# Performance work log

Measured on AMD Instinct MI355X. Metric: run time of the kernel, lower is better.

Reference implementation:

```python
import jax, jax.numpy as jnp
import numpy as np


def setup_inputs() -> dict:
    key = jax.random.key(0)
    k0, k1, k2, k3, k4, k5 = jax.random.split(key, 6)
    L1, L2, B, D = 512, 512, 32, 1024
    inputs1 = jax.random.normal(k0, (L1, B, D), dtype=jnp.float32)
    inputs2 = jax.random.normal(k1, (L2, B, D), dtype=jnp.float32)
    # mask value 0 marks a valid token (module keeps pairs where both masks == 0)
    mask1 = jax.random.randint(k2, (L1, B), 0, 2, dtype=jnp.int64)
    mask2 = jax.random.randint(k3, (L2, B), 0, 2, dtype=jnp.int64)
    W = jax.random.normal(k4, (D, D), dtype=jnp.float32) * 0.02
    b = jax.random.normal(k5, (1,), dtype=jnp.float32) * 0.02
    return {"inputs1": inputs1, "inputs2": inputs2, "mask1": mask1,
            "mask2": mask2, "W": W, "b": b, "k": 256}


def reference(inputs1, inputs2, mask1, mask2, W, b, k):
    # inputs: [len, bsz, hdim]; masks: [len, bsz]
    H1 = jnp.transpose(inputs1, (1, 0, 2))  # [B, L1, D]
    H2 = jnp.transpose(inputs2, (1, 0, 2))  # [B, L2, D]
    # bilinear scores: H1 @ W @ H2^T + b, then relu  -> [B, L1, L2]
    S = jax.nn.relu(jnp.einsum('bid,de,bje->bij', H1, W, H2) + b[0])
    # pair is valid iff both mask entries are 0
    valid = (mask1.T[:, :, None] == 0) & (mask2.T[:, None, :] == 0)  # [B, L1, L2]
    B = S.shape[0]
    S_flat = jnp.where(valid.reshape(B, -1), S.reshape(B, -1), -jnp.inf)
    num_elems = S_flat.shape[1]
    k_actual = min(k, num_elems)
    q, _ = jax.lax.top_k(S_flat, k_actual)  # [B, k_actual]
    # replace -inf tail entries with the last finite value in each row
    neg = jnp.isneginf(q)
    q_num_finite = k_actual - neg.sum(axis=-1)  # [B]
    fill = jnp.take_along_axis(q, (q_num_finite - 1)[:, None], axis=1)  # [B, 1]
    q = jnp.where(neg, fill, q)
    if k_actual < k:
        q = jnp.concatenate(
            [q, jnp.broadcast_to(q[:, -1:], (B, k - k_actual))], axis=1)
    return q
```

## Files before the change

kernel.cpp:

```cpp
#include <hip/hip_runtime.h>

typedef __bf16 bf16_t;
typedef bf16_t bf16x8 __attribute__((ext_vector_type(8)));
typedef float floatx4 __attribute__((ext_vector_type(4)));

#define L1C 512
#define L2C 512
#define BC  32
#define DC  1024
#define KTOP 256
#define NBIN 4096
#define CAP  1024
#define FBUF 16384

__device__ __forceinline__ unsigned short f2bf(float f) {
    unsigned u = __float_as_uint(f);
    u += 0x7FFFu + ((u >> 16) & 1u);
    return (unsigned short)(u >> 16);
}

__device__ __forceinline__ void g2l16(const unsigned short* g, unsigned short* l) {
    __builtin_amdgcn_global_load_lds((const unsigned int*)g, (unsigned int*)l,
                                     16, 0, 0);
}

__device__ __forceinline__ float decode_key(unsigned k) {
    return __uint_as_float(k & 0x7FFFFFFFu);
}

__global__ __launch_bounds__(256) void cast_tr_kernel(
    const float* __restrict__ in1, const float* __restrict__ in2,
    unsigned short* __restrict__ A1, unsigned short* __restrict__ A2) {
    int r = blockIdx.x;
    const float* src;
    unsigned short* dst;
    if (r < L1C * BC) {
        int l = r >> 5, b = r & 31;
        src = in1 + (size_t)r * DC;
        dst = A1 + ((size_t)b * L1C + l) * DC;
    } else {
        int r2 = r - L1C * BC;
        int l = r2 >> 5, b = r2 & 31;
        src = in2 + (size_t)r2 * DC;
        dst = A2 + ((size_t)b * L2C + l) * DC;
    }
    int t = threadIdx.x;
    float4 v = reinterpret_cast<const float4*>(src)[t];
    ushort4 o;
    o.x = f2bf(v.x); o.y = f2bf(v.y); o.z = f2bf(v.z); o.w = f2bf(v.w);
    reinterpret_cast<ushort4*>(dst)[t] = o;
}

__global__ void transpose_cast_kernel(const float* __restrict__ W,
                                      unsigned short* __restrict__ Wt) {
    __shared__ float tile[32][33];
    int d0 = blockIdx.x * 32, e0 = blockIdx.y * 32;
    int tx = threadIdx.x;
    for (int i = threadIdx.y; i < 32; i += 8)
        tile[i][tx] = W[(size_t)(d0 + i) * DC + e0 + tx];
    __syncthreads();
    for (int i = threadIdx.y; i < 32; i += 8)
        Wt[(size_t)(e0 + i) * DC + d0 + tx] = f2bf(tile[tx][i]);
}

__global__ void init_kernel(const int* __restrict__ mask1,
                            const int* __restrict__ mask2,
                            int* __restrict__ m1t, int* __restrict__ m2t,
                            unsigned* __restrict__ cnt) {
    int gid = blockIdx.x * blockDim.x + threadIdx.x;
    if (gid < L1C * BC) {
        int l = gid & 511, b = gid >> 9;
        m1t[gid] = mask1[(l << 5) + b];
        m2t[gid] = mask2[(l << 5) + b];
    }
    if (gid < BC * 16) cnt[gid] = 0;
}

__global__ __launch_bounds__(256) void gemm1_kernel(
    const unsigned short* __restrict__ A,
    const unsigned short* __restrict__ Bt,
    unsigned short* __restrict__ C) {
    __shared__ unsigned short As[128][32];
    __shared__ unsigned short Bs[128][32];
    int tid = threadIdx.x;
    int wave = tid >> 6, lane = tid & 63;
    int lane15 = lane & 15, quad = lane >> 4;
    int wm = wave >> 1, wn = wave & 1;
    size_t m0 = (size_t)blockIdx.x * 128, n0 = (size_t)blockIdx.y * 128;

    floatx4 zero = {0.f, 0.f, 0.f, 0.f};
    floatx4 acc[4][4];
#pragma unroll
    for (int i = 0; i < 4; i++)
#pragma unroll
        for (int j = 0; j < 4; j++) acc[i][j] = zero;

    for (int k0 = 0; k0 < DC; k0 += 32) {
#pragma unroll
        for (int c = 0; c < 2; c++) {
            int cid = c * 256 + tid;
            int row = cid >> 2, col8 = (cid & 3) * 8;
            unsigned short* lbase = &As[0][0] + (c * 256 + wave * 64) * 8;
            g2l16(&A[(m0 + row) * DC + k0 + col8], lbase);
            unsigned short* lbase2 = &Bs[0][0] + (c * 256 + wave * 64) * 8;
            g2l16(&Bt[(n0 + row) * DC + k0 + col8], lbase2);
        }
        __syncthreads();
        bf16x8 af[4], bfr[4];
#pragma unroll
        for (int mi = 0; mi < 4; mi++)
            af[mi] = *reinterpret_cast<const bf16x8*>(&As[wm * 64 + mi * 16 + lane15][quad * 8]);
#pragma unroll
        for (int ni = 0; ni < 4; ni++)
            bfr[ni] = *reinterpret_cast<const bf16x8*>(&Bs[wn * 64 + ni * 16 + lane15][quad * 8]);
#pragma unroll
        for (int mi = 0; mi < 4; mi++)
#pragma unroll
            for (int ni = 0; ni < 4; ni++)
                acc[mi][ni] = __builtin_amdgcn_mfma_f32_16x16x32_bf16(
                    af[mi], bfr[ni], acc[mi][ni], 0, 0, 0);
        __syncthreads();
    }
#pragma unroll
    for (int mi = 0; mi < 4; mi++)
#pragma unroll
        for (int ni = 0; ni < 4; ni++)
#pragma unroll
            for (int r = 0; r < 4; r++) {
                size_t row = m0 + wm * 64 + mi * 16 + quad * 4 + r;
                size_t col = n0 + wn * 64 + ni * 16 + lane15;
                C[row * DC + col] = f2bf(acc[mi][ni][r]);
            }
}

__global__ __launch_bounds__(256) void gemm2_kernel(
    const unsigned short* __restrict__ Tm,
    const unsigned short* __restrict__ H2,
    const int* __restrict__ m1t, const int* __restrict__ m2t,
    const float* __restrict__ bptr,
    unsigned* __restrict__ cand,
    unsigned* __restrict__ cnt) {
    __shared__ unsigned short As[128][32];
    __shared__ unsigned short Bs[128][32];
    __shared__ unsigned lh[NBIN];
    __shared__ unsigned csum[256];
    __shared__ int m1s[128], m2s[128];
    __shared__ unsigned tsh, lcnt;
    int tid = threadIdx.x;
    int wave = tid >> 6, lane = tid & 63;
    int lane15 = lane & 15, quad = lane >> 4;
    int wm = wave >> 1, wn = wave & 1;
    int L = blockIdx.x;
    int xcd = L & 7, tile = (L >> 3) & 15, chunk = L >> 7;
    int b = xcd + (chunk << 3);
    int bx = tile & 3, by = tile >> 2;
    int m0 = bx * 128, n0 = by * 128;
    int gblk = b * 16 + by * 4 + bx;
    const unsigned short* Ab = Tm + (size_t)b * L1C * DC;
    const unsigned short* Bb = H2 + (size_t)b * L2C * DC;

    for (int i = tid; i < NBIN; i += 256) lh[i] = 0;
    if (tid < 128) m1s[tid] = (m1t[b * L1C + m0 + tid] == 0);
    else           m2s[tid - 128] = (m2t[b * L2C + n0 + tid - 128] == 0);

    floatx4 zero = {0.f, 0.f, 0.f, 0.f};
    floatx4 acc[4][4];
#pragma unroll
    for (int i = 0; i < 4; i++)
#pragma unroll
        for (int j = 0; j < 4; j++) acc[i][j] = zero;

    for (int k0 = 0; k0 < DC; k0 += 32) {
#pragma unroll
        for (int c = 0; c < 2; c++) {
            int cid = c * 256 + tid;
            int row = cid >> 2, col8 = (cid & 3) * 8;
            unsigned short* lbase = &As[0][0] + (c * 256 + wave * 64) * 8;
            g2l16(&Ab[(size_t)(m0 + row) * DC + k0 + col8], lbase);
            unsigned short* lbase2 = &Bs[0][0] + (c * 256 + wave * 64) * 8;
            g2l16(&Bb[(size_t)(n0 + row) * DC + k0 + col8], lbase2);
        }
        __syncthreads();
        bf16x8 af[4], bfr[4];
#pragma unroll
        for (int mi = 0; mi < 4; mi++)
            af[mi] = *reinterpret_cast<const bf16x8*>(&As[wm * 64 + mi * 16 + lane15][quad * 8]);
#pragma unroll
        for (int ni = 0; ni < 4; ni++)
            bfr[ni] = *reinterpret_cast<const bf16x8*>(&Bs[wn * 64 + ni * 16 + lane15][quad * 8]);
#pragma unroll
        for (int mi = 0; mi < 4; mi++)
#pragma unroll
            for (int ni = 0; ni < 4; ni++)
                acc[mi][ni] = __builtin_amdgcn_mfma_f32_16x16x32_bf16(
                    af[mi], bfr[ni], acc[mi][ni], 0, 0, 0);
        __syncthreads();
    }

    float bias = bptr[0];
    unsigned zc = 0;
#pragma unroll
    for (int ni = 0; ni < 4; ni++) {
        int jl = wn * 64 + ni * 16 + lane15;
        int v2 = m2s[jl];
#pragma unroll
        for (int mi = 0; mi < 4; mi++)
#pragma unroll
            for (int r = 0; r < 4; r++) {
                int il = wm * 64 + mi * 16 + quad * 4 + r;
                float s = acc[mi][ni][r] + bias;
                if (v2 && m1s[il]) {
                    if (s > 0.f)
                        atomicAdd(&lh[(__float_as_uint(s) | 0x80000000u) >> 20], 1u);
                    else
                        zc++;
                }
            }
    }
    if (zc) atomicAdd(&lh[2048], zc);
    __syncthreads();
    unsigned s16 = 0;
#pragma unroll
    for (int i = 0; i < 16; i++) s16 += lh[tid * 16 + i];
    csum[tid] = s16;
    __syncthreads();
    if (tid == 0) {
        unsigned cum = 0, bin = 2048;
        int found = 0;
        for (int c = 255; c >= 128 && !found; --c) {
            unsigned cs = csum[c];
            if (cum + cs >= KTOP) {
                for (int bb = c * 16 + 15; bb >= c * 16; --bb) {
                    unsigned h = lh[bb];
                    if (cum + h >= KTOP) { bin = (unsigned)bb; found = 1; break; }
                    cum += h;
                }
            } else cum += cs;
        }
        tsh = bin << 20;
        lcnt = 0;
    }
    __syncthreads();
    unsigned T = tsh;
    unsigned base = (unsigned)gblk * CAP;
#pragma unroll
    for (int ni = 0; ni < 4; ni++) {
        int jl = wn * 64 + ni * 16 + lane15;
        int v2 = m2s[jl];
#pragma unroll
        for (int mi = 0; mi < 4; mi++)
#pragma unroll
            for (int r = 0; r < 4; r++) {
                int il = wm * 64 + mi * 16 + quad * 4 + r;
                float s = acc[mi][ni][r] + bias;
                s = s > 0.f ? s : 0.f;
                unsigned key = (v2 && m1s[il])
                                   ? (__float_as_uint(s) | 0x80000000u) : 0u;
                if (key >= T) {
                    unsigned p = atomicAdd(&lcnt, 1u);
                    if (p < CAP) cand[base + p] = key;
                }
            }
    }
    __syncthreads();
    if (tid == 0) cnt[gblk] = lcnt < CAP ? lcnt : CAP;
}

__global__ __launch_bounds__(1024) void final_kernel(
    const unsigned* __restrict__ cand, const unsigned* __restrict__ cnt,
    float* __restrict__ out) {
    __shared__ unsigned buf[FBUF];
    __shared__ unsigned h[NBIN];
    __shared__ unsigned ss[256];
    __shared__ unsigned scnt_s[16], off_s[16];
    __shared__ unsigned ntot_s, sel_c, sel_a, B_s, R_s, mcount;
    __shared__ int have_s;
    __shared__ unsigned srt[256];
    int b = blockIdx.x, tid = threadIdx.x;

    if (tid < 16) {
        unsigned c = cnt[b * 16 + tid];
        scnt_s[tid] = c < CAP ? c : CAP;
    }
    __syncthreads();
    if (tid == 0) {
        unsigned o = 0;
        for (int i = 0; i < 16; i++) { off_s[i] = o; o += scnt_s[i]; }
        ntot_s = o;
        have_s = 1;
    }
    __syncthreads();
    for (int blk = 0; blk < 16; blk++) {
        unsigned c = scnt_s[blk], o = off_s[blk];
        const unsigned* p = cand + (size_t)(b * 16 + blk) * CAP;
        for (unsigned i = tid; i < c; i += 1024) buf[o + i] = p[i];
    }
    __syncthreads();
    unsigned n = ntot_s;

    unsigned Kr = KTOP;
    unsigned pfx = 0;
    unsigned kth = 0;
    for (int pass = 0; pass < 3; pass++) {
        int bins = (pass < 2) ? NBIN : 256;
        int shift = (pass == 0) ? 20 : (pass == 1) ? 8 : 0;
        int nch = bins >> 4;
        for (int i = tid; i < bins; i += 1024) h[i] = 0;
        __syncthreads();
        for (unsigned i = tid; i < n; i += 1024) {
            unsigned k = buf[i];
            bool ok = (pass == 0) ||
                      (pass == 1 && (k >> 20) == pfx) ||
                      (pass == 2 && (k >> 8) == pfx);
            if (ok) atomicAdd(&h[(k >> shift) & (bins - 1)], 1u);
        }
        __syncthreads();
        if (tid < nch) {
            unsigned s = 0;
#pragma unroll
            for (int i = 0; i < 16; i++) s += h[tid * 16 + i];
            ss[tid] = s;
        }
        __syncthreads();
        for (int off = 1; off < nch; off <<= 1) {
            unsigned v = 0;
            if (tid < nch && tid + (unsigned)off < (unsigned)nch) v = ss[tid + off];
            __syncthreads();
            if (tid < nch) ss[tid] += v;
            __syncthreads();
        }
        if (pass == 0) {
            if (tid == 0) have_s = (ss[0] >= KTOP);
            __syncthreads();
            if (!have_s) break;
        }
        if (tid < nch) {
            unsigned above = (tid + 1 < (unsigned)nch) ? ss[tid + 1] : 0u;
            if (above < Kr && ss[tid] >= Kr) { sel_c = tid; sel_a = above; }
        }
        __syncthreads();
        if (tid == 0) {
            unsigned cum = sel_a;
            for (int bb = (int)sel_c * 16 + 15; bb >= (int)sel_c * 16; --bb) {
                unsigned hb = h[bb];
                if (cum + hb >= Kr) { B_s = (unsigned)bb; R_s = Kr - cum; break; }
                cum += hb;
            }
        }
        __syncthreads();
        unsigned Bv = B_s;
        Kr = R_s;
        if (pass == 0) pfx = Bv;
        else if (pass == 1) pfx = (pfx << 12) | Bv;
        else kth = (pfx << 8) | Bv;
        __syncthreads();
    }

    if (tid == 0) mcount = 0;
    __syncthreads();
    int have = have_s;
    unsigned lim = have ? kth : 0u;
    for (unsigned i = tid; i < n; i += 1024) {
        unsigned k = buf[i];
        if (k > lim) {
            unsigned p = atomicAdd(&mcount, 1u);
            if (p < 256) srt[p] = k;
        }
    }
    __syncthreads();
    unsigned m = mcount;
    if (tid < 256 && tid >= (int)m) srt[tid] = have ? kth : 0u;
    for (int k2 = 2; k2 <= 256; k2 <<= 1) {
        for (int j2 = k2 >> 1; j2 > 0; j2 >>= 1) {
            __syncthreads();
            if (tid < 256) {
                int ixj = tid ^ j2;
                if (ixj > tid) {
                    unsigned a = srt[tid], c = srt[ixj];
                    bool up = (tid & k2) == 0;
                    if (up ? (a < c) : (a > c)) { srt[tid] = c; srt[ixj] = a; }
                }
            }
        }
    }
    __syncthreads();
    if (tid < 256) {
        unsigned nval = have ? KTOP : (m < KTOP ? m : KTOP);
        float v;
        if ((unsigned)tid < nval) v = decode_key(srt[tid]);
        else v = (nval > 0) ? decode_key(srt[nval - 1]) : -__builtin_inff();
        out[b * KTOP + tid] = v;
    }
}

extern "C" void kernel_launch(void* const* d_in, const int* in_sizes, int n_in,
                              void* d_out, int out_size, void* d_ws, size_t ws_size,
                              hipStream_t stream) {
    const float* in1   = (const float*)d_in[0];
    const float* in2   = (const float*)d_in[1];
    const int*   mask1 = (const int*)d_in[2];
    const int*   mask2 = (const int*)d_in[3];
    const float* W     = (const float*)d_in[4];
    const float* bias  = (const float*)d_in[5];
    float* out = (float*)d_out;

    char* ws = (char*)d_ws;
    size_t off = 0;
    const size_t nElem = (size_t)L1C * BC * DC;
    unsigned short* A1 = (unsigned short*)(ws + off); off += nElem * 2;
    unsigned short* A2 = (unsigned short*)(ws + off); off += nElem * 2;
    unsigned short* Wt = (unsigned short*)(ws + off); off += (size_t)DC * DC * 2;
    unsigned short* Tm = (unsigned short*)(ws + off); off += nElem * 2;
    unsigned* cand = (unsigned*)(ws + off); off += (size_t)BC * 16 * CAP * 4;
    unsigned* cnt  = (unsigned*)(ws + off); off += (size_t)BC * 16 * 4;
    int* m1t = (int*)(ws + off); off += (size_t)BC * L1C * 4;
    int* m2t = (int*)(ws + off); off += (size_t)BC * L2C * 4;

    cast_tr_kernel<<<2 * L1C * BC, 256, 0, stream>>>(in1, in2, A1, A2);
    transpose_cast_kernel<<<dim3(DC / 32, DC / 32), dim3(32, 8), 0, stream>>>(W, Wt);
    init_kernel<<<64, 256, 0, stream>>>(mask1, mask2, m1t, m2t, cnt);

    gemm1_kernel<<<dim3(128, 8), 256, 0, stream>>>(A1, Wt, Tm);
    gemm2_kernel<<<512, 256, 0, stream>>>(Tm, A2, m1t, m2t, bias, cand, cnt);
    final_kernel<<<BC, 1024, 0, stream>>>(cand, cnt, out);
}
```

Measured before the change: 281.1 us.

## Reassociate bilinear product as H2·Wᵀ, fuse prep kernels, deepen GEMM1 K-tile

```diff
diff --git a/kernel.cpp b/kernel.cpp
--- a/kernel.cpp
+++ b/kernel.cpp
@@ -28,60 +28,51 @@
     return __uint_as_float(k & 0x7FFFFFFFu);
 }
 
-__global__ __launch_bounds__(256) void cast_tr_kernel(
+__global__ __launch_bounds__(256) void prep_kernel(
     const float* __restrict__ in1, const float* __restrict__ in2,
-    unsigned short* __restrict__ A1, unsigned short* __restrict__ A2) {
-    int r = blockIdx.x;
-    const float* src;
-    unsigned short* dst;
-    if (r < L1C * BC) {
-        int l = r >> 5, b = r & 31;
-        src = in1 + (size_t)r * DC;
-        dst = A1 + ((size_t)b * L1C + l) * DC;
+    const float* __restrict__ W,
+    const int* __restrict__ mask1, const int* __restrict__ mask2,
+    unsigned short* __restrict__ A1, unsigned short* __restrict__ A2,
+    unsigned short* __restrict__ Wb,
+    int* __restrict__ m1t, int* __restrict__ m2t,
+    unsigned* __restrict__ cnt) {
+    int r = blockIdx.x, t = threadIdx.x;
+    if (r < 2 * L1C * BC + DC) {
+        const float* src;
+        unsigned short* dst;
+        if (r < L1C * BC) {
+            int l = r >> 5, b = r & 31;
+            src = in1 + (size_t)r * DC;
+            dst = A1 + ((size_t)b * L1C + l) * DC;
+        } else if (r < 2 * L1C * BC) {
+            int r2 = r - L1C * BC;
+            int l = r2 >> 5, b = r2 & 31;
+            src = in2 + (size_t)r2 * DC;
+            dst = A2 + ((size_t)b * L2C + l) * DC;
+        } else {
+            int r3 = r - 2 * L1C * BC;
+            src = W + (size_t)r3 * DC;
+            dst = Wb + (size_t)r3 * DC;
+        }
+        float4 v = reinterpret_cast<const float4*>(src)[t];
+        ushort4 o;
+        o.x = f2bf(v.x); o.y = f2bf(v.y); o.z = f2bf(v.z); o.w = f2bf(v.w);
+        reinterpret_cast<ushort4*>(dst)[t] = o;
     } else {
-        int r2 = r - L1C * BC;
-        int l = r2 >> 5, b = r2 & 31;
-        src = in2 + (size_t)r2 * DC;
-        dst = A2 + ((size_t)b * L2C + l) * DC;
-    }
-    int t = threadIdx.x;
-    float4 v = reinterpret_cast<const float4*>(src)[t];
-    ushort4 o;
-    o.x = f2bf(v.x); o.y = f2bf(v.y); o.z = f2bf(v.z); o.w = f2bf(v.w);
-    reinterpret_cast<ushort4*>(dst)[t] = o;
-}
-
-__global__ void transpose_cast_kernel(const float* __restrict__ W,
-                                      unsigned short* __restrict__ Wt) {
-    __shared__ float tile[32][33];
-    int d0 = blockIdx.x * 32, e0 = blockIdx.y * 32;
-    int tx = threadIdx.x;
-    for (int i = threadIdx.y; i < 32; i += 8)
-        tile[i][tx] = W[(size_t)(d0 + i) * DC + e0 + tx];
-    __syncthreads();
-    for (int i = threadIdx.y; i < 32; i += 8)
-        Wt[(size_t)(e0 + i) * DC + d0 + tx] = f2bf(tile[tx][i]);
-}
-
-__global__ void init_kernel(const int* __restrict__ mask1,
-                            const int* __restrict__ mask2,
-                            int* __restrict__ m1t, int* __restrict__ m2t,
-                            unsigned* __restrict__ cnt) {
-    int gid = blockIdx.x * blockDim.x + threadIdx.x;
-    if (gid < L1C * BC) {
+        int gid = (r - (2 * L1C * BC + DC)) * 256 + t;
         int l = gid & 511, b = gid >> 9;
         m1t[gid] = mask1[(l << 5) + b];
         m2t[gid] = mask2[(l << 5) + b];
-    }
-    if (gid < BC * 16) cnt[gid] = 0;
+        if (gid < BC * 16) cnt[gid] = 0;
+    }
 }
 
 __global__ __launch_bounds__(256) void gemm1_kernel(
     const unsigned short* __restrict__ A,
     const unsigned short* __restrict__ Bt,
     unsigned short* __restrict__ C) {
-    __shared__ unsigned short As[128][32];
-    __shared__ unsigned short Bs[128][32];
+    __shared__ unsigned short As[128][64];
+    __shared__ unsigned short Bs[128][64];
     int tid = threadIdx.x;
     int wave = tid >> 6, lane = tid & 63;
     int lane15 = lane & 15, quad = lane >> 4;
@@ -95,30 +86,35 @@
 #pragma unroll
         for (int j = 0; j < 4; j++) acc[i][j] = zero;
 
-    for (int k0 = 0; k0 < DC; k0 += 32) {
-#pragma unroll
-        for (int c = 0; c < 2; c++) {
+    for (int k0 = 0; k0 < DC; k0 += 64) {
+#pragma unroll
+        for (int c = 0; c < 4; c++) {
             int cid = c * 256 + tid;
-            int row = cid >> 2, col8 = (cid & 3) * 8;
+            int row = cid >> 3, col8 = (cid & 7) * 8;
             unsigned short* lbase = &As[0][0] + (c * 256 + wave * 64) * 8;
             g2l16(&A[(m0 + row) * DC + k0 + col8], lbase);
             unsigned short* lbase2 = &Bs[0][0] + (c * 256 + wave * 64) * 8;
             g2l16(&Bt[(n0 + row) * DC + k0 + col8], lbase2);
         }
         __syncthreads();
-        bf16x8 af[4], bfr[4];
-#pragma unroll
-        for (int mi = 0; mi < 4; mi++)
-            af[mi] = *reinterpret_cast<const bf16x8*>(&As[wm * 64 + mi * 16 + lane15][quad * 8]);
-#pragma unroll
-        for (int ni = 0; ni < 4; ni++)
-            bfr[ni] = *reinterpret_cast<const bf16x8*>(&Bs[wn * 64 + ni * 16 + lane15][quad * 8]);
-#pragma unroll
-        for (int mi = 0; mi < 4; mi++)
+#pragma unroll
+        for (int kk = 0; kk < 64; kk += 32) {
+            bf16x8 af[4], bfr[4];
+#pragma unroll
+            for (int mi = 0; mi < 4; mi++)
+                af[mi] = *reinterpret_cast<const bf16x8*>(
+                    &As[wm * 64 + mi * 16 + lane15][kk + quad * 8]);
 #pragma unroll
             for (int ni = 0; ni < 4; ni++)
-                acc[mi][ni] = __builtin_amdgcn_mfma_f32_16x16x32_bf16(
-                    af[mi], bfr[ni], acc[mi][ni], 0, 0, 0);
+                bfr[ni] = *reinterpret_cast<const bf16x8*>(
+                    &Bs[wn * 64 + ni * 16 + lane15][kk + quad * 8]);
+#pragma unroll
+            for (int mi = 0; mi < 4; mi++)
+#pragma unroll
+                for (int ni = 0; ni < 4; ni++)
+                    acc[mi][ni] = __builtin_amdgcn_mfma_f32_16x16x32_bf16(
+                        af[mi], bfr[ni], acc[mi][ni], 0, 0, 0);
+        }
         __syncthreads();
     }
 #pragma unroll
@@ -134,8 +130,8 @@
 }
 
 __global__ __launch_bounds__(256) void gemm2_kernel(
-    const unsigned short* __restrict__ Tm,
-    const unsigned short* __restrict__ H2,
+    const unsigned short* __restrict__ A1,
+    const unsigned short* __restrict__ V,
     const int* __restrict__ m1t, const int* __restrict__ m2t,
     const float* __restrict__ bptr,
     unsigned* __restrict__ cand,
@@ -156,8 +152,8 @@
     int bx = tile & 3, by = tile >> 2;
     int m0 = bx * 128, n0 = by * 128;
     int gblk = b * 16 + by * 4 + bx;
-    const unsigned short* Ab = Tm + (size_t)b * L1C * DC;
-    const unsigned short* Bb = H2 + (size_t)b * L2C * DC;
+    const unsigned short* Ab = A1 + (size_t)b * L1C * DC;
+    const unsigned short* Bb = V + (size_t)b * L2C * DC;
 
     for (int i = tid; i < NBIN; i += 256) lh[i] = 0;
     if (tid < 128) m1s[tid] = (m1t[b * L1C + m0 + tid] == 0);
@@ -277,6 +273,7 @@
     __shared__ int have_s;
     __shared__ unsigned srt[256];
     int b = blockIdx.x, tid = threadIdx.x;
+    int wv = tid >> 6, ln = tid & 63;
 
     if (tid < 16) {
         unsigned c = cnt[b * 16 + tid];
@@ -290,10 +287,10 @@
         have_s = 1;
     }
     __syncthreads();
-    for (int blk = 0; blk < 16; blk++) {
-        unsigned c = scnt_s[blk], o = off_s[blk];
-        const unsigned* p = cand + (size_t)(b * 16 + blk) * CAP;
-        for (unsigned i = tid; i < c; i += 1024) buf[o + i] = p[i];
+    {
+        unsigned c = scnt_s[wv], o = off_s[wv];
+        const unsigned* p = cand + (size_t)(b * 16 + wv) * CAP;
+        for (unsigned i = ln; i < c; i += 64) buf[o + i] = p[i];
     }
     __syncthreads();
     unsigned n = ntot_s;
@@ -409,18 +406,16 @@
     const size_t nElem = (size_t)L1C * BC * DC;
     unsigned short* A1 = (unsigned short*)(ws + off); off += nElem * 2;
     unsigned short* A2 = (unsigned short*)(ws + off); off += nElem * 2;
-    unsigned short* Wt = (unsigned short*)(ws + off); off += (size_t)DC * DC * 2;
-    unsigned short* Tm = (unsigned short*)(ws + off); off += nElem * 2;
+    unsigned short* Wb = (unsigned short*)(ws + off); off += (size_t)DC * DC * 2;
+    unsigned short* V  = (unsigned short*)(ws + off); off += nElem * 2;
     unsigned* cand = (unsigned*)(ws + off); off += (size_t)BC * 16 * CAP * 4;
     unsigned* cnt  = (unsigned*)(ws + off); off += (size_t)BC * 16 * 4;
     int* m1t = (int*)(ws + off); off += (size_t)BC * L1C * 4;
     int* m2t = (int*)(ws + off); off += (size_t)BC * L2C * 4;
 
-    cast_tr_kernel<<<2 * L1C * BC, 256, 0, stream>>>(in1, in2, A1, A2);
-    transpose_cast_kernel<<<dim3(DC / 32, DC / 32), dim3(32, 8), 0, stream>>>(W, Wt);
-    init_kernel<<<64, 256, 0, stream>>>(mask1, mask2, m1t, m2t, cnt);
-
-    gemm1_kernel<<<dim3(128, 8), 256, 0, stream>>>(A1, Wt, Tm);
-    gemm2_kernel<<<512, 256, 0, stream>>>(Tm, A2, m1t, m2t, bias, cand, cnt);
+    prep_kernel<<<2 * L1C * BC + DC + 64, 256, 0, stream>>>(
+        in1, in2, W, mask1, mask2, A1, A2, Wb, m1t, m2t, cnt);
+    gemm1_kernel<<<dim3(128, 8), 256, 0, stream>>>(A2, Wb, V);
+    gemm2_kernel<<<512, 256, 0, stream>>>(A1, V, m1t, m2t, bias, cand, cnt);
     final_kernel<<<BC, 1024, 0, stream>>>(cand, cnt, out);
 }
```

New measurement: 275.2 us. 1.02x faster.
